# Performance work log

Measured on AMD Instinct MI355X. Metric: run time of the kernel, lower is better.

The kernel has to match this reference:

```python
import jax, jax.numpy as jnp
import numpy as np

N_HEADS = 12
C = 3          # per-head in/hidden/out channels (12/4)
C_PRED = 1     # predictor hidden (4/4)
BN_EPS = 1e-5
COS_EPS = 1e-8
B, H, W = 8, 512, 768


def setup_inputs() -> dict:
    key = jax.random.key(0)
    ks = jax.random.split(key, 22)
    p = lambda k, s: jax.random.normal(k, s, jnp.float32) * 0.1
    return {
        "latent1": jax.random.normal(ks[0], (B, N_HEADS, H, W), jnp.float32),
        "latent2": jax.random.normal(ks[1], (B, N_HEADS, H, W), jnp.float32),
        # projector conv1 + BN
        "W1": p(ks[2], (N_HEADS, C, C)), "b1": p(ks[3], (N_HEADS, C)),
        "g1": 1.0 + p(ks[4], (N_HEADS, C)), "be1": p(ks[5], (N_HEADS, C)),
        # projector conv2 + BN
        "W2": p(ks[6], (N_HEADS, C, C)), "b2": p(ks[7], (N_HEADS, C)),
        "g2": 1.0 + p(ks[8], (N_HEADS, C)), "be2": p(ks[9], (N_HEADS, C)),
        # projector conv3 + BN (no ReLU)
        "W3": p(ks[10], (N_HEADS, C, C)), "b3": p(ks[11], (N_HEADS, C)),
        "g3": 1.0 + p(ks[12], (N_HEADS, C)), "be3": p(ks[13], (N_HEADS, C)),
        # predictor conv1 + BN
        "W4": p(ks[14], (N_HEADS, C_PRED, C)), "b4": p(ks[15], (N_HEADS, C_PRED)),
        "g4": 1.0 + p(ks[16], (N_HEADS, C_PRED)), "be4": p(ks[17], (N_HEADS, C_PRED)),
        # predictor conv2 (no BN)
        "W5": p(ks[18], (N_HEADS, C, C_PRED)), "b5": p(ks[19], (N_HEADS, C)),
    }


def _conv1x1(x, Wk, bk):
    # x: [B, Cin, H, W'], Wk: [Cout, Cin]
    return jnp.einsum('oc,bchw->bohw', Wk, x) + bk[None, :, None, None]


def _bn(x, g, be):
    # training-mode BatchNorm2d: batch statistics over (B, H, W)
    m = x.mean(axis=(0, 2, 3), keepdims=True)
    v = x.var(axis=(0, 2, 3), keepdims=True)  # biased var, as torch BN uses
    return (x - m) * jax.lax.rsqrt(v + BN_EPS) * g[None, :, None, None] + be[None, :, None, None]


def _cos_loss(p, z):
    # -mean(cosine_similarity(p, detach(z), dim=1))
    z = jax.lax.stop_gradient(z)
    dot = jnp.sum(p * z, axis=1)
    npn = jnp.maximum(jnp.sqrt(jnp.sum(p * p, axis=1)), COS_EPS)
    nzn = jnp.maximum(jnp.sqrt(jnp.sum(z * z, axis=1)), COS_EPS)
    return -jnp.mean(dot / (npn * nzn))


def _head_loss(x1, x2, W1, b1, g1, be1, W2, b2, g2, be2, W3, b3, g3, be3,
               W4, b4, g4, be4, W5, b5):
    def proj(x):
        x = jax.nn.relu(_bn(_conv1x1(x, W1, b1), g1, be1))
        x = jax.nn.relu(_bn(_conv1x1(x, W2, b2), g2, be2))
        return _bn(_conv1x1(x, W3, b3), g3, be3)

    def pred(z):
        h = jax.nn.relu(_bn(_conv1x1(z, W4, b4), g4, be4))
        return _conv1x1(h, W5, b5)

    z1, z2 = proj(x1), proj(x2)
    p1, p2 = pred(z1), pred(z2)
    return 0.5 * (_cos_loss(p1, z2) + _cos_loss(p2, z1))


def reference(latent1, latent2, W1, b1, g1, be1, W2, b2, g2, be2,
              W3, b3, g3, be3, W4, b4, g4, be4, W5, b5):
    Bd, Cd, Hd, Wd = latent1.shape
    Wp = Wd // C
    # per-channel view [B, H, W] -> [B, 3, H, W/3]; stack heads on leading axis
    x1 = latent1.reshape(Bd, N_HEADS, C, Hd, Wp).transpose(1, 0, 2, 3, 4)
    x2 = latent2.reshape(Bd, N_HEADS, C, Hd, Wp).transpose(1, 0, 2, 3, 4)
    losses = jax.vmap(_head_loss)(x1, x2, W1, b1, g1, be1, W2, b2, g2, be2,
                                  W3, b3, g3, be3, W4, b4, g4, be4, W5, b5)
    return jnp.sum(losses)
```

## Files before the change

### kernel.cpp

```cpp
#include <hip/hip_runtime.h>
#include <hip/hip_fp16.h>
#include <math.h>


typedef unsigned short ushort_t;
typedef unsigned int   uint_t;

constexpr int   NH      = 12;
constexpr int   POS     = 131072;
constexpr int   NB      = 8;
constexpr long long MLL = (long long)NB * POS;
constexpr int   CSPAN   = POS / 16;
constexpr int   SBLK    = 128;
constexpr int   NTOT    = NB * NH * 3 * POS;

constexpr size_t XH_BYTES   = (size_t)NTOT * 2;
constexpr size_t P_CNT      = (size_t)24 * SBLK * 9;
constexpr size_t DBL_COUNT  = 3 * P_CNT + (size_t)12 * SBLK;
constexpr size_t NEED_BYTES = 2 * XH_BYTES + DBL_COUNT * 8 + (size_t)24 * 40 * 4;

template <int K>
__device__ inline void block_reduce_to0(double (&v)[K]) {
#pragma unroll
  for (int off = 32; off > 0; off >>= 1) {
#pragma unroll
    for (int k = 0; k < K; ++k) v[k] += __shfl_down(v[k], off, 64);
  }
  __shared__ double lds[4][K];
  const int lane = threadIdx.x & 63;
  const int wv   = threadIdx.x >> 6;
  if (lane == 0) {
#pragma unroll
    for (int k = 0; k < K; ++k) lds[wv][k] = v[k];
  }
  __syncthreads();
  if (threadIdx.x == 0) {
#pragma unroll
    for (int k = 0; k < K; ++k) v[k] = lds[0][k] + lds[1][k] + lds[2][k] + lds[3][k];
  }
}

__device__ inline uint_t pack2h(float lo, float hi) {
  return (uint_t)__half_as_ushort(__float2half(lo)) |
         ((uint_t)__half_as_ushort(__float2half(hi)) << 16);
}
__device__ inline float h_lo(uint_t w) {
  return __half2float(__ushort_as_half((unsigned short)(w & 0xFFFFu)));
}
__device__ inline float h_hi(uint_t w) {
  return __half2float(__ushort_as_half((unsigned short)(w >> 16)));
}

template <bool H16>
__device__ inline void load3x8(const float* __restrict__ X,
                               const ushort_t* __restrict__ XH,
                               size_t e, float (&f)[3][8]) {
#pragma unroll
  for (int c = 0; c < 3; ++c) {
    const size_t a = e + (size_t)c * POS;
    if constexpr (H16) {
      const uint4 v = *(const uint4*)(XH + a);
      f[c][0] = h_lo(v.x); f[c][1] = h_hi(v.x);
      f[c][2] = h_lo(v.y); f[c][3] = h_hi(v.y);
      f[c][4] = h_lo(v.z); f[c][5] = h_hi(v.z);
      f[c][6] = h_lo(v.w); f[c][7] = h_hi(v.w);
    } else {
      const float4 u0 = *(const float4*)(X + a);
      const float4 u1 = *(const float4*)(X + a + 4);
      f[c][0] = u0.x; f[c][1] = u0.y; f[c][2] = u0.z; f[c][3] = u0.w;
      f[c][4] = u1.x; f[c][5] = u1.y; f[c][6] = u1.z; f[c][7] = u1.w;
    }
  }
}

__device__ inline void store8h(ushort_t* __restrict__ XH, size_t e,
                               const float (&g)[8]) {
  uint4 h;
  h.x = pack2h(g[0], g[1]);
  h.y = pack2h(g[2], g[3]);
  h.z = pack2h(g[4], g[5]);
  h.w = pack2h(g[6], g[7]);
  *(uint4*)(XH + e) = h;
}

template <bool STORE>
__global__ __launch_bounds__(256) void passA1_kernel(
    const float* __restrict__ x1, const float* __restrict__ x2,
    ushort_t* __restrict__ xh1, ushort_t* __restrict__ xh2,
    double* __restrict__ P0) {
  const int u = blockIdx.y;
  const int s = u % 24;
  const int b = u / 24;
  const int n = s >> 1;
  const float* __restrict__ X = (s & 1) ? x2 : x1;
  ushort_t* __restrict__ XH = (s & 1) ? xh2 : xh1;
  const size_t off0 = (size_t)((b * NH + n) * 3) * POS + (size_t)blockIdx.x * CSPAN;

  float acc[9] = {0.f, 0.f, 0.f, 0.f, 0.f, 0.f, 0.f, 0.f, 0.f};
#pragma unroll 2
  for (int i = 0; i < 4; ++i) {
    const size_t e = off0 + i * 2048 + threadIdx.x * 8;
    float f[3][8];
    load3x8<false>(X, nullptr, e, f);
    if constexpr (STORE) {
#pragma unroll
      for (int c = 0; c < 3; ++c) store8h(XH, e + (size_t)c * POS, f[c]);
    }
#pragma unroll
    for (int j = 0; j < 8; ++j) {
      const float X0 = f[0][j], X1 = f[1][j], X2 = f[2][j];
      acc[0] += X0;      acc[1] += X1;      acc[2] += X2;
      acc[3] += X0 * X0; acc[4] += X1 * X1; acc[5] += X2 * X2;
      acc[6] += X0 * X1; acc[7] += X0 * X2; acc[8] += X1 * X2;
    }
  }

  double v9[9];
#pragma unroll
  for (int k = 0; k < 9; ++k) v9[k] = (double)acc[k];
  block_reduce_to0<9>(v9);
  if (threadIdx.x == 0) {
    double* dst = P0 + ((size_t)s * SBLK + b * 16 + blockIdx.x) * 9;
#pragma unroll
    for (int k = 0; k < 9; ++k) dst[k] = v9[k];
  }
}

__device__ inline void moments_to_mc(const double (&v)[9], double (&m)[3],
                                     double (&C)[3][3]) {
  const double M = (double)MLL;
  m[0] = v[0] / M; m[1] = v[1] / M; m[2] = v[2] / M;
  C[0][0] = v[3] / M - m[0] * m[0];
  C[1][1] = v[4] / M - m[1] * m[1];
  C[2][2] = v[5] / M - m[2] * m[2];
  C[0][1] = C[1][0] = v[6] / M - m[0] * m[1];
  C[0][2] = C[2][0] = v[7] / M - m[0] * m[2];
  C[1][2] = C[2][1] = v[8] / M - m[1] * m[2];
}

__global__ __launch_bounds__(256) void stats_fold_kernel(
    const double* __restrict__ P, const float* __restrict__ Wk,
    const float* __restrict__ bk, const float* __restrict__ gk,
    const float* __restrict__ bek, float* __restrict__ derived, int outoff) {
  const int s = blockIdx.x;
  const int t = threadIdx.x;
  const int n = s >> 1;
  double v[9] = {0, 0, 0, 0, 0, 0, 0, 0, 0};
  if (t < SBLK) {
    const double* p = P + ((size_t)s * SBLK + t) * 9;
#pragma unroll
    for (int k = 0; k < 9; ++k) v[k] = p[k];
  }
  block_reduce_to0<9>(v);
  if (t == 0) {
    double m[3], C[3][3];
    moments_to_mc(v, m, C);
    for (int o = 0; o < 3; ++o) {
      const double w0 = Wk[n * 9 + o * 3 + 0];
      const double w1 = Wk[n * 9 + o * 3 + 1];
      const double w2 = Wk[n * 9 + o * 3 + 2];
      const double my = w0 * m[0] + w1 * m[1] + w2 * m[2] + (double)bk[n * 3 + o];
      const double vy = w0 * w0 * C[0][0] + w1 * w1 * C[1][1] + w2 * w2 * C[2][2] +
                        2.0 * (w0 * w1 * C[0][1] + w0 * w2 * C[0][2] + w1 * w2 * C[1][2]);
      const double sc = (double)gk[n * 3 + o] / sqrt(vy + 1e-5);
      const double tt = (double)bek[n * 3 + o] - my * sc;
      derived[s * 40 + outoff + o * 3 + 0] = (float)(sc * w0);
      derived[s * 40 + outoff + o * 3 + 1] = (float)(sc * w1);
      derived[s * 40 + outoff + o * 3 + 2] = (float)(sc * w2);
      derived[s * 40 + outoff + 9 + o]     = (float)(sc * (double)bk[n * 3 + o] + tt);
    }
  }
}

template <bool H16>
__global__ __launch_bounds__(256) void passA2_kernel(
    const float* __restrict__ x1, const float* __restrict__ x2,
    ushort_t* __restrict__ xh1, ushort_t* __restrict__ xh2,
    const float* __restrict__ derived, double* __restrict__ P1) {
  const int u = blockIdx.y;
  const int s = u % 24;
  const int b = u / 24;
  const int n = s >> 1;
  const float* __restrict__ X = (s & 1) ? x2 : x1;
  ushort_t* __restrict__ XH = (s & 1) ? xh2 : xh1;
  const size_t off0 = (size_t)((b * NH + n) * 3) * POS + (size_t)blockIdx.x * CSPAN;

  const float* D = derived + s * 40;
  float w1f[3][3], c1v[3];
#pragma unroll
  for (int o = 0; o < 3; ++o) {
#pragma unroll
    for (int c = 0; c < 3; ++c) w1f[o][c] = D[o * 3 + c];
    c1v[o] = D[9 + o];
  }

  float acc[9] = {0.f, 0.f, 0.f, 0.f, 0.f, 0.f, 0.f, 0.f, 0.f};
#pragma unroll 2
  for (int i = 0; i < 4; ++i) {
    const size_t e = off0 + i * 2048 + threadIdx.x * 8;
    float f[3][8];
    load3x8<H16>(X, XH, e, f);
    float A[3][8];
#pragma unroll
    for (int j = 0; j < 8; ++j) {
      const float X0 = f[0][j], X1 = f[1][j], X2 = f[2][j];
#pragma unroll
      for (int o = 0; o < 3; ++o)
        A[o][j] = fmaxf(0.f, fmaf(w1f[o][0], X0,
                         fmaf(w1f[o][1], X1, fmaf(w1f[o][2], X2, c1v[o]))));
      const float A0 = A[0][j], A1 = A[1][j], A2v = A[2][j];
      acc[0] += A0;       acc[1] += A1;       acc[2] += A2v;
      acc[3] += A0 * A0;  acc[4] += A1 * A1;  acc[5] += A2v * A2v;
      acc[6] += A0 * A1;  acc[7] += A0 * A2v; acc[8] += A1 * A2v;
    }
    if constexpr (H16) {
#pragma unroll
      for (int c = 0; c < 3; ++c) store8h(XH, e + (size_t)c * POS, A[c]);
    }
  }

  double v9[9];
#pragma unroll
  for (int k = 0; k < 9; ++k) v9[k] = (double)acc[k];
  block_reduce_to0<9>(v9);
  if (threadIdx.x == 0) {
    double* dst = P1 + ((size_t)s * SBLK + b * 16 + blockIdx.x) * 9;
#pragma unroll
    for (int k = 0; k < 9; ++k) dst[k] = v9[k];
  }
}

template <bool H16>
__global__ __launch_bounds__(256) void passC2_kernel(
    const float* __restrict__ x1, const float* __restrict__ x2,
    ushort_t* __restrict__ xh1, ushort_t* __restrict__ xh2,
    const float* __restrict__ derived, double* __restrict__ P2) {
  const int u = blockIdx.y;
  const int s = u % 24;
  const int b = u / 24;
  const int n = s >> 1;
  const float* __restrict__ X = (s & 1) ? x2 : x1;
  ushort_t* __restrict__ XH = (s & 1) ? xh2 : xh1;
  const size_t off0 = (size_t)((b * NH + n) * 3) * POS + (size_t)blockIdx.x * CSPAN;

  const float* D = derived + s * 40;
  float w1f[3][3], c1v[3];
  if constexpr (!H16) {
#pragma unroll
    for (int o = 0; o < 3; ++o) {
#pragma unroll
      for (int c = 0; c < 3; ++c) w1f[o][c] = D[o * 3 + c];
      c1v[o] = D[9 + o];
    }
  }
  float w2f[3][3], c2v[3];
#pragma unroll
  for (int o = 0; o < 3; ++o) {
#pragma unroll
    for (int c = 0; c < 3; ++c) w2f[o][c] = D[12 + o * 3 + c];
    c2v[o] = D[21 + o];
  }

  float acc[9] = {0.f, 0.f, 0.f, 0.f, 0.f, 0.f, 0.f, 0.f, 0.f};
#pragma unroll 2
  for (int i = 0; i < 4; ++i) {
    const size_t e = off0 + i * 2048 + threadIdx.x * 8;
    float f[3][8];
    load3x8<H16>(X, XH, e, f);
    float A[3][8];
#pragma unroll
    for (int j = 0; j < 8; ++j) {
      float a0, a1, a2;
      if constexpr (H16) {
        a0 = f[0][j]; a1 = f[1][j]; a2 = f[2][j];
      } else {
        const float X0 = f[0][j], X1 = f[1][j], X2 = f[2][j];
        a0 = fmaxf(0.f, fmaf(w1f[0][0], X0, fmaf(w1f[0][1], X1, fmaf(w1f[0][2], X2, c1v[0]))));
        a1 = fmaxf(0.f, fmaf(w1f[1][0], X0, fmaf(w1f[1][1], X1, fmaf(w1f[1][2], X2, c1v[1]))));
        a2 = fmaxf(0.f, fmaf(w1f[2][0], X0, fmaf(w1f[2][1], X1, fmaf(w1f[2][2], X2, c1v[2]))));
      }
#pragma unroll
      for (int o = 0; o < 3; ++o)
        A[o][j] = fmaxf(0.f, fmaf(w2f[o][0], a0,
                         fmaf(w2f[o][1], a1, fmaf(w2f[o][2], a2, c2v[o]))));
      const float A0 = A[0][j], A1 = A[1][j], A2v = A[2][j];
      acc[0] += A0;       acc[1] += A1;       acc[2] += A2v;
      acc[3] += A0 * A0;  acc[4] += A1 * A1;  acc[5] += A2v * A2v;
      acc[6] += A0 * A1;  acc[7] += A0 * A2v; acc[8] += A1 * A2v;
    }
    if constexpr (H16) {
#pragma unroll
      for (int c = 0; c < 3; ++c) store8h(XH, e + (size_t)c * POS, A[c]);
    }
  }

  double v9[9];
#pragma unroll
  for (int k = 0; k < 9; ++k) v9[k] = (double)acc[k];
  block_reduce_to0<9>(v9);
  if (threadIdx.x == 0) {
    double* dst = P2 + ((size_t)s * SBLK + b * 16 + blockIdx.x) * 9;
#pragma unroll
    for (int k = 0; k < 9; ++k) dst[k] = v9[k];
  }
}

__global__ __launch_bounds__(256) void statsC2_kernel(
    const double* __restrict__ P2, const float* __restrict__ W3,
    const float* __restrict__ b3, const float* __restrict__ g3,
    const float* __restrict__ be3, const float* __restrict__ W4,
    const float* __restrict__ b4, const float* __restrict__ g4,
    const float* __restrict__ be4, float* __restrict__ derived) {
  const int s = blockIdx.x;
  const int t = threadIdx.x;
  const int n = s >> 1;
  double v[9] = {0, 0, 0, 0, 0, 0, 0, 0, 0};
  if (t < SBLK) {
    const double* p = P2 + ((size_t)s * SBLK + t) * 9;
#pragma unroll
    for (int k = 0; k < 9; ++k) v[k] = p[k];
  }
  block_reduce_to0<9>(v);
  if (t == 0) {
    double m[3], C[3][3];
    moments_to_mc(v, m, C);
    double F3d[3][3], c3d[3];
    for (int o = 0; o < 3; ++o) {
      const double w0 = W3[n * 9 + o * 3 + 0];
      const double w1 = W3[n * 9 + o * 3 + 1];
      const double w2 = W3[n * 9 + o * 3 + 2];
      const double m3 = w0 * m[0] + w1 * m[1] + w2 * m[2] + (double)b3[n * 3 + o];
      const double vy = w0 * w0 * C[0][0] + w1 * w1 * C[1][1] + w2 * w2 * C[2][2] +
                        2.0 * (w0 * w1 * C[0][1] + w0 * w2 * C[0][2] + w1 * w2 * C[1][2]);
      const double s3 = (double)g3[n * 3 + o] / sqrt(vy + 1e-5);
      const double t3 = (double)be3[n * 3 + o] - m3 * s3;
      F3d[o][0] = s3 * w0; F3d[o][1] = s3 * w1; F3d[o][2] = s3 * w2;
      c3d[o] = s3 * (double)b3[n * 3 + o] + t3;
      derived[s * 40 + 24 + o * 3 + 0] = (float)F3d[o][0];
      derived[s * 40 + 24 + o * 3 + 1] = (float)F3d[o][1];
      derived[s * 40 + 24 + o * 3 + 2] = (float)F3d[o][2];
      derived[s * 40 + 33 + o]         = (float)c3d[o];
    }
    double q[3] = {0.0, 0.0, 0.0};
    double d = (double)b4[n];
    for (int o = 0; o < 3; ++o) {
      const double w4o = W4[n * 3 + o];
      q[0] += w4o * F3d[o][0];
      q[1] += w4o * F3d[o][1];
      q[2] += w4o * F3d[o][2];
      d += w4o * c3d[o];
    }
    const double m4 = q[0] * m[0] + q[1] * m[1] + q[2] * m[2] + d;
    double v4 = 0.0;
    for (int i2 = 0; i2 < 3; ++i2)
      for (int j2 = 0; j2 < 3; ++j2) v4 += q[i2] * q[j2] * C[i2][j2];
    const double s4 = (double)g4[n] / sqrt(v4 + 1e-5);
    const double t4 = (double)be4[n] - m4 * s4;
    for (int o = 0; o < 3; ++o)
      derived[s * 40 + 36 + o] = (float)(s4 * (double)W4[n * 3 + o]);
    derived[s * 40 + 39] = (float)(s4 * (double)b4[n] + t4);
  }
}

template <bool H16>
__device__ inline void tail_chain(
    const float (&F1)[3][3], const float (&C1)[3],
    const float (&F2)[3][3], const float (&C2)[3],
    const float (&F3)[3][3], const float (&C3)[3],
    const float (&W4s)[3], float B4c,
    const float (&w5)[3], const float (&b5v)[3],
    float v0, float v1, float v2, float (&z)[3], float (&p)[3]) {
  float a0 = v0, a1 = v1, a2 = v2;
  if constexpr (!H16) {
    const float t0 = fmaxf(0.f, fmaf(F1[0][0], v0, fmaf(F1[0][1], v1, fmaf(F1[0][2], v2, C1[0]))));
    const float t1 = fmaxf(0.f, fmaf(F1[1][0], v0, fmaf(F1[1][1], v1, fmaf(F1[1][2], v2, C1[1]))));
    const float t2 = fmaxf(0.f, fmaf(F1[2][0], v0, fmaf(F1[2][1], v1, fmaf(F1[2][2], v2, C1[2]))));
    a0 = fmaxf(0.f, fmaf(F2[0][0], t0, fmaf(F2[0][1], t1, fmaf(F2[0][2], t2, C2[0]))));
    a1 = fmaxf(0.f, fmaf(F2[1][0], t0, fmaf(F2[1][1], t1, fmaf(F2[1][2], t2, C2[1]))));
    a2 = fmaxf(0.f, fmaf(F2[2][0], t0, fmaf(F2[2][1], t1, fmaf(F2[2][2], t2, C2[2]))));
  }
#pragma unroll
  for (int o = 0; o < 3; ++o)
    z[o] = fmaf(F3[o][0], a0, fmaf(F3[o][1], a1, fmaf(F3[o][2], a2, C3[o])));
  const float y4 = fmaf(W4s[0], z[0], fmaf(W4s[1], z[1], fmaf(W4s[2], z[2], B4c)));
  const float h = fmaxf(0.f, y4);
#pragma unroll
  for (int o = 0; o < 3; ++o) p[o] = fmaf(w5[o], h, b5v[o]);
}

template <bool H16>
__global__ __launch_bounds__(256) void passD2_kernel(
    const float* __restrict__ x1, const float* __restrict__ x2,
    const ushort_t* __restrict__ xh1, const ushort_t* __restrict__ xh2,
    const float* __restrict__ W5, const float* __restrict__ b5,
    const float* __restrict__ derived, double* __restrict__ PL) {
  const int u = blockIdx.y;
  const int n = u % 12;
  const int b = u / 12;
  const size_t off0 = (size_t)((b * NH + n) * 3) * POS + (size_t)blockIdx.x * CSPAN;

  float F1[2][3][3], C1[2][3], F2[2][3][3], C2[2][3];
  float F3[2][3][3], C3[2][3], W4s[2][3], B4c[2];
#pragma unroll
  for (int br = 0; br < 2; ++br) {
    const float* D = derived + (size_t)(2 * n + br) * 40;
    if constexpr (!H16) {
#pragma unroll
      for (int o = 0; o < 3; ++o) {
#pragma unroll
        for (int c = 0; c < 3; ++c) {
          F1[br][o][c] = D[o * 3 + c];
          F2[br][o][c] = D[12 + o * 3 + c];
        }
        C1[br][o] = D[9 + o];
        C2[br][o] = D[21 + o];
      }
    }
#pragma unroll
    for (int o = 0; o < 3; ++o) {
#pragma unroll
      for (int c = 0; c < 3; ++c) F3[br][o][c] = D[24 + o * 3 + c];
      C3[br][o]  = D[33 + o];
      W4s[br][o] = D[36 + o];
    }
    B4c[br] = D[39];
  }
  float w5[3], b5v[3];
#pragma unroll
  for (int o = 0; o < 3; ++o) {
    w5[o]  = W5[n * 3 + o];
    b5v[o] = b5[n * 3 + o];
  }

  float acc = 0.f;
  for (int i = 0; i < 4; ++i) {
    const size_t e = off0 + i * 2048 + threadIdx.x * 8;
    float fA[3][8], fB[3][8];
    load3x8<H16>(x1, xh1, e, fA);
    load3x8<H16>(x2, xh2, e, fB);
#pragma unroll
    for (int j = 0; j < 8; ++j) {
      float z1[3], p1[3], z2[3], p2[3];
      tail_chain<H16>(F1[0], C1[0], F2[0], C2[0], F3[0], C3[0], W4s[0], B4c[0],
                      w5, b5v, fA[0][j], fA[1][j], fA[2][j], z1, p1);
      tail_chain<H16>(F1[1], C1[1], F2[1], C2[1], F3[1], C3[1], W4s[1], B4c[1],
                      w5, b5v, fB[0][j], fB[1][j], fB[2][j], z2, p2);

      const float d12 = p1[0] * z2[0] + p1[1] * z2[1] + p1[2] * z2[2];
      const float pp1 = p1[0] * p1[0] + p1[1] * p1[1] + p1[2] * p1[2];
      const float zz2 = z2[0] * z2[0] + z2[1] * z2[1] + z2[2] * z2[2];
      acc += d12 * __builtin_amdgcn_rsqf(fmaxf(pp1, 1e-16f)) *
                   __builtin_amdgcn_rsqf(fmaxf(zz2, 1e-16f));

      const float d21 = p2[0] * z1[0] + p2[1] * z1[1] + p2[2] * z1[2];
      const float pp2 = p2[0] * p2[0] + p2[1] * p2[1] + p2[2] * p2[2];
      const float zz1 = z1[0] * z1[0] + z1[1] * z1[1] + z1[2] * z1[2];
      acc += d21 * __builtin_amdgcn_rsqf(fmaxf(pp2, 1e-16f)) *
                   __builtin_amdgcn_rsqf(fmaxf(zz1, 1e-16f));
    }
  }

  double v[1] = {(double)acc};
  block_reduce_to0<1>(v);
  if (threadIdx.x == 0) PL[(size_t)n * SBLK + b * 16 + blockIdx.x] = v[0];
}

__global__ __launch_bounds__(256) void finalize_kernel(
    const double* __restrict__ PL, float* __restrict__ out) {
  double v[1] = {0.0};
  for (int k = threadIdx.x; k < 12 * SBLK; k += 256) v[0] += PL[k];
  block_reduce_to0<1>(v);
  if (threadIdx.x == 0) out[0] = (float)(-0.5 * v[0] / (double)MLL);
}

extern "C" void kernel_launch(void* const* d_in, const int* in_sizes, int n_in,
                              void* d_out, int out_size, void* d_ws, size_t ws_size,
                              hipStream_t stream) {
  const float* x1  = (const float*)d_in[0];
  const float* x2  = (const float*)d_in[1];
  const float* W1  = (const float*)d_in[2];
  const float* b1  = (const float*)d_in[3];
  const float* g1  = (const float*)d_in[4];
  const float* be1 = (const float*)d_in[5];
  const float* W2  = (const float*)d_in[6];
  const float* b2  = (const float*)d_in[7];
  const float* g2  = (const float*)d_in[8];
  const float* be2 = (const float*)d_in[9];
  const float* W3  = (const float*)d_in[10];
  const float* b3  = (const float*)d_in[11];
  const float* g3  = (const float*)d_in[12];
  const float* be3 = (const float*)d_in[13];
  const float* W4  = (const float*)d_in[14];
  const float* b4  = (const float*)d_in[15];
  const float* g4  = (const float*)d_in[16];
  const float* be4 = (const float*)d_in[17];
  const float* W5  = (const float*)d_in[18];
  const float* b5  = (const float*)d_in[19];

  const bool big = ws_size >= NEED_BYTES;
  ushort_t* xh1 = nullptr;
  ushort_t* xh2 = nullptr;
  double* dbase;
  if (big) {
    xh1 = (ushort_t*)d_ws;
    xh2 = xh1 + NTOT;
    dbase = (double*)(xh2 + NTOT);
  } else {
    dbase = (double*)d_ws;
  }
  double* P0 = dbase;
  double* P1 = P0 + P_CNT;
  double* P2 = P1 + P_CNT;
  double* PL = P2 + P_CNT;
  float* derived = (float*)(PL + 12 * SBLK);

  const dim3 blk(256);
  const dim3 gA(16, 192);
  const dim3 gD(16, 96);

  if (big) {
    passA1_kernel<true><<<gA, blk, 0, stream>>>(x1, x2, xh1, xh2, P0);
    stats_fold_kernel<<<24, blk, 0, stream>>>(P0, W1, b1, g1, be1, derived, 0);
    passA2_kernel<true><<<gA, blk, 0, stream>>>(x1, x2, xh1, xh2, derived, P1);
    stats_fold_kernel<<<24, blk, 0, stream>>>(P1, W2, b2, g2, be2, derived, 12);
    passC2_kernel<true><<<gA, blk, 0, stream>>>(x1, x2, xh1, xh2, derived, P2);
    statsC2_kernel<<<24, blk, 0, stream>>>(P2, W3, b3, g3, be3, W4, b4, g4, be4,
                                           derived);
    passD2_kernel<true><<<gD, blk, 0, stream>>>(x1, x2, xh1, xh2, W5, b5,
                                                derived, PL);
  } else {
    passA1_kernel<false><<<gA, blk, 0, stream>>>(x1, x2, nullptr, nullptr, P0);
    stats_fold_kernel<<<24, blk, 0, stream>>>(P0, W1, b1, g1, be1, derived, 0);
    passA2_kernel<false><<<gA, blk, 0, stream>>>(x1, x2, nullptr, nullptr,
                                                 derived, P1);
    stats_fold_kernel<<<24, blk, 0, stream>>>(P1, W2, b2, g2, be2, derived, 12);
    passC2_kernel<false><<<gA, blk, 0, stream>>>(x1, x2, nullptr, nullptr,
                                                 derived, P2);
    statsC2_kernel<<<24, blk, 0, stream>>>(P2, W3, b3, g3, be3, W4, b4, g4, be4,
                                           derived);
    passD2_kernel<false><<<gD, blk, 0, stream>>>(x1, x2, nullptr, nullptr, W5, b5,
                                                 derived, PL);
  }
  finalize_kernel<<<1, blk, 0, stream>>>(PL, (float*)d_out);
}
```

Measured before the change: 505.8 us.

## Fold BN statistics into pass prologues and drop intermediate fp16 activation writes

Removes the separate stats-fold kernels and the finalize kernel. Each pass now reduces the previous per-block moment partials and computes the folded BN affine in its own prologue, and the last pass accumulates the loss with atomics plus a last-block counter. Later passes no longer write fp16 intermediate activations; they recompute the full chain from the fp16 copy of the input. This trades fewer launches and less write traffic for redundant prologue reductions in every block and extra ALU work recomputing earlier layers.

```diff
diff --git a/kernel.cpp b/kernel.cpp
--- a/kernel.cpp
+++ b/kernel.cpp
@@ -14,10 +14,8 @@
 constexpr int   SBLK    = 128;
 constexpr int   NTOT    = NB * NH * 3 * POS;
 
-constexpr size_t XH_BYTES   = (size_t)NTOT * 2;
 constexpr size_t P_CNT      = (size_t)24 * SBLK * 9;
-constexpr size_t DBL_COUNT  = 3 * P_CNT + (size_t)12 * SBLK;
-constexpr size_t NEED_BYTES = 2 * XH_BYTES + DBL_COUNT * 8 + (size_t)24 * 40 * 4;
+constexpr size_t NEED_BYTES = (size_t)NTOT * 2 * 2 + 3 * P_CNT * 8 + 64;
 
 template <int K>
 __device__ inline void block_reduce_to0(double (&v)[K]) {
@@ -27,6 +25,7 @@
     for (int k = 0; k < K; ++k) v[k] += __shfl_down(v[k], off, 64);
   }
   __shared__ double lds[4][K];
+  __syncthreads();
   const int lane = threadIdx.x & 63;
   const int wv   = threadIdx.x >> 6;
   if (lane == 0) {
@@ -83,49 +82,6 @@
   *(uint4*)(XH + e) = h;
 }
 
-template <bool STORE>
-__global__ __launch_bounds__(256) void passA1_kernel(
-    const float* __restrict__ x1, const float* __restrict__ x2,
-    ushort_t* __restrict__ xh1, ushort_t* __restrict__ xh2,
-    double* __restrict__ P0) {
-  const int u = blockIdx.y;
-  const int s = u % 24;
-  const int b = u / 24;
-  const int n = s >> 1;
-  const float* __restrict__ X = (s & 1) ? x2 : x1;
-  ushort_t* __restrict__ XH = (s & 1) ? xh2 : xh1;
-  const size_t off0 = (size_t)((b * NH + n) * 3) * POS + (size_t)blockIdx.x * CSPAN;
-
-  float acc[9] = {0.f, 0.f, 0.f, 0.f, 0.f, 0.f, 0.f, 0.f, 0.f};
-#pragma unroll 2
-  for (int i = 0; i < 4; ++i) {
-    const size_t e = off0 + i * 2048 + threadIdx.x * 8;
-    float f[3][8];
-    load3x8<false>(X, nullptr, e, f);
-    if constexpr (STORE) {
-#pragma unroll
-      for (int c = 0; c < 3; ++c) store8h(XH, e + (size_t)c * POS, f[c]);
-    }
-#pragma unroll
-    for (int j = 0; j < 8; ++j) {
-      const float X0 = f[0][j], X1 = f[1][j], X2 = f[2][j];
-      acc[0] += X0;      acc[1] += X1;      acc[2] += X2;
-      acc[3] += X0 * X0; acc[4] += X1 * X1; acc[5] += X2 * X2;
-      acc[6] += X0 * X1; acc[7] += X0 * X2; acc[8] += X1 * X2;
-    }
-  }
-
-  double v9[9];
-#pragma unroll
-  for (int k = 0; k < 9; ++k) v9[k] = (double)acc[k];
-  block_reduce_to0<9>(v9);
-  if (threadIdx.x == 0) {
-    double* dst = P0 + ((size_t)s * SBLK + b * 16 + blockIdx.x) * 9;
-#pragma unroll
-    for (int k = 0; k < 9; ++k) dst[k] = v9[k];
-  }
-}
-
 __device__ inline void moments_to_mc(const double (&v)[9], double (&m)[3],
                                      double (&C)[3][3]) {
   const double M = (double)MLL;
@@ -138,45 +94,98 @@
   C[1][2] = C[2][1] = v[8] / M - m[1] * m[2];
 }
 
-__global__ __launch_bounds__(256) void stats_fold_kernel(
-    const double* __restrict__ P, const float* __restrict__ Wk,
-    const float* __restrict__ bk, const float* __restrict__ gk,
-    const float* __restrict__ bek, float* __restrict__ derived, int outoff) {
-  const int s = blockIdx.x;
-  const int t = threadIdx.x;
-  const int n = s >> 1;
-  double v[9] = {0, 0, 0, 0, 0, 0, 0, 0, 0};
-  if (t < SBLK) {
-    const double* p = P + ((size_t)s * SBLK + t) * 9;
+__device__ inline void slice_reduce9(const double* __restrict__ P, int s,
+                                     double (&v)[9]) {
+#pragma unroll
+  for (int k = 0; k < 9; ++k) v[k] = 0.0;
+  if (threadIdx.x < SBLK) {
+    const double* p = P + ((size_t)s * SBLK + threadIdx.x) * 9;
 #pragma unroll
     for (int k = 0; k < 9; ++k) v[k] = p[k];
   }
   block_reduce_to0<9>(v);
-  if (t == 0) {
-    double m[3], C[3][3];
-    moments_to_mc(v, m, C);
-    for (int o = 0; o < 3; ++o) {
-      const double w0 = Wk[n * 9 + o * 3 + 0];
-      const double w1 = Wk[n * 9 + o * 3 + 1];
-      const double w2 = Wk[n * 9 + o * 3 + 2];
-      const double my = w0 * m[0] + w1 * m[1] + w2 * m[2] + (double)bk[n * 3 + o];
-      const double vy = w0 * w0 * C[0][0] + w1 * w1 * C[1][1] + w2 * w2 * C[2][2] +
-                        2.0 * (w0 * w1 * C[0][1] + w0 * w2 * C[0][2] + w1 * w2 * C[1][2]);
-      const double sc = (double)gk[n * 3 + o] / sqrt(vy + 1e-5);
-      const double tt = (double)bek[n * 3 + o] - my * sc;
-      derived[s * 40 + outoff + o * 3 + 0] = (float)(sc * w0);
-      derived[s * 40 + outoff + o * 3 + 1] = (float)(sc * w1);
-      derived[s * 40 + outoff + o * 3 + 2] = (float)(sc * w2);
-      derived[s * 40 + outoff + 9 + o]     = (float)(sc * (double)bk[n * 3 + o] + tt);
-    }
-  }
-}
-
-template <bool H16>
-__global__ __launch_bounds__(256) void passA2_kernel(
+}
+
+__device__ inline void fold_math(const double (&v)[9], const float* __restrict__ Wk,
+                                 const float* __restrict__ bk,
+                                 const float* __restrict__ gk,
+                                 const float* __restrict__ bek, int n,
+                                 float* __restrict__ dst) {
+  double m[3], C[3][3];
+  moments_to_mc(v, m, C);
+  for (int o = 0; o < 3; ++o) {
+    const double w0 = Wk[n * 9 + o * 3 + 0];
+    const double w1 = Wk[n * 9 + o * 3 + 1];
+    const double w2 = Wk[n * 9 + o * 3 + 2];
+    const double my = w0 * m[0] + w1 * m[1] + w2 * m[2] + (double)bk[n * 3 + o];
+    const double vy = w0 * w0 * C[0][0] + w1 * w1 * C[1][1] + w2 * w2 * C[2][2] +
+                      2.0 * (w0 * w1 * C[0][1] + w0 * w2 * C[0][2] + w1 * w2 * C[1][2]);
+    const double sc = (double)gk[n * 3 + o] / sqrt(vy + 1e-5);
+    const double tt = (double)bek[n * 3 + o] - my * sc;
+    dst[o * 3 + 0] = (float)(sc * w0);
+    dst[o * 3 + 1] = (float)(sc * w1);
+    dst[o * 3 + 2] = (float)(sc * w2);
+    dst[9 + o]     = (float)(sc * (double)bk[n * 3 + o] + tt);
+  }
+}
+
+__device__ inline void fold34_math(const double (&v)[9], const float* __restrict__ W3,
+                                   const float* __restrict__ b3,
+                                   const float* __restrict__ g3,
+                                   const float* __restrict__ be3,
+                                   const float* __restrict__ W4,
+                                   const float* __restrict__ b4,
+                                   const float* __restrict__ g4,
+                                   const float* __restrict__ be4, int n,
+                                   float* __restrict__ dst) {
+  double m[3], C[3][3];
+  moments_to_mc(v, m, C);
+  double F3d[3][3], c3d[3];
+  for (int o = 0; o < 3; ++o) {
+    const double w0 = W3[n * 9 + o * 3 + 0];
+    const double w1 = W3[n * 9 + o * 3 + 1];
+    const double w2 = W3[n * 9 + o * 3 + 2];
+    const double m3 = w0 * m[0] + w1 * m[1] + w2 * m[2] + (double)b3[n * 3 + o];
+    const double vy = w0 * w0 * C[0][0] + w1 * w1 * C[1][1] + w2 * w2 * C[2][2] +
+                      2.0 * (w0 * w1 * C[0][1] + w0 * w2 * C[0][2] + w1 * w2 * C[1][2]);
+    const double s3 = (double)g3[n * 3 + o] / sqrt(vy + 1e-5);
+    const double t3 = (double)be3[n * 3 + o] - m3 * s3;
+    F3d[o][0] = s3 * w0; F3d[o][1] = s3 * w1; F3d[o][2] = s3 * w2;
+    c3d[o] = s3 * (double)b3[n * 3 + o] + t3;
+    dst[o * 3 + 0] = (float)F3d[o][0];
+    dst[o * 3 + 1] = (float)F3d[o][1];
+    dst[o * 3 + 2] = (float)F3d[o][2];
+    dst[9 + o]     = (float)c3d[o];
+  }
+  double q[3] = {0.0, 0.0, 0.0};
+  double d = (double)b4[n];
+  for (int o = 0; o < 3; ++o) {
+    const double w4o = W4[n * 3 + o];
+    q[0] += w4o * F3d[o][0];
+    q[1] += w4o * F3d[o][1];
+    q[2] += w4o * F3d[o][2];
+    d += w4o * c3d[o];
+  }
+  const double m4 = q[0] * m[0] + q[1] * m[1] + q[2] * m[2] + d;
+  double v4 = 0.0;
+  for (int i = 0; i < 3; ++i)
+    for (int j = 0; j < 3; ++j) v4 += q[i] * q[j] * C[i][j];
+  const double s4 = (double)g4[n] / sqrt(v4 + 1e-5);
+  const double t4 = (double)be4[n] - m4 * s4;
+  for (int o = 0; o < 3; ++o) dst[12 + o] = (float)(s4 * (double)W4[n * 3 + o]);
+  dst[15] = (float)(s4 * (double)b4[n] + t4);
+}
+
+template <bool STORE>
+__global__ __launch_bounds__(256) void pass1_kernel(
     const float* __restrict__ x1, const float* __restrict__ x2,
     ushort_t* __restrict__ xh1, ushort_t* __restrict__ xh2,
-    const float* __restrict__ derived, double* __restrict__ P1) {
+    double* __restrict__ P0, double* __restrict__ lossAcc,
+    uint_t* __restrict__ cnt) {
+  if (blockIdx.x == 0 && blockIdx.y == 0 && threadIdx.x == 0) {
+    *lossAcc = 0.0;
+    *cnt = 0u;
+  }
   const int u = blockIdx.y;
   const int s = u % 24;
   const int b = u / 24;
@@ -185,13 +194,63 @@
   ushort_t* __restrict__ XH = (s & 1) ? xh2 : xh1;
   const size_t off0 = (size_t)((b * NH + n) * 3) * POS + (size_t)blockIdx.x * CSPAN;
 
-  const float* D = derived + s * 40;
+  float acc[9] = {0.f, 0.f, 0.f, 0.f, 0.f, 0.f, 0.f, 0.f, 0.f};
+#pragma unroll 2
+  for (int i = 0; i < 4; ++i) {
+    const size_t e = off0 + i * 2048 + threadIdx.x * 8;
+    float f[3][8];
+    load3x8<false>(X, nullptr, e, f);
+    if constexpr (STORE) {
+#pragma unroll
+      for (int c = 0; c < 3; ++c) store8h(XH, e + (size_t)c * POS, f[c]);
+    }
+#pragma unroll
+    for (int j = 0; j < 8; ++j) {
+      const float X0 = f[0][j], X1 = f[1][j], X2 = f[2][j];
+      acc[0] += X0;      acc[1] += X1;      acc[2] += X2;
+      acc[3] += X0 * X0; acc[4] += X1 * X1; acc[5] += X2 * X2;
+      acc[6] += X0 * X1; acc[7] += X0 * X2; acc[8] += X1 * X2;
+    }
+  }
+  double v9[9];
+#pragma unroll
+  for (int k = 0; k < 9; ++k) v9[k] = (double)acc[k];
+  block_reduce_to0<9>(v9);
+  if (threadIdx.x == 0) {
+    double* dst = P0 + ((size_t)s * SBLK + b * 16 + blockIdx.x) * 9;
+#pragma unroll
+    for (int k = 0; k < 9; ++k) dst[k] = v9[k];
+  }
+}
+
+template <bool H16>
+__global__ __launch_bounds__(256) void pass2_kernel(
+    const float* __restrict__ x1, const float* __restrict__ x2,
+    const ushort_t* __restrict__ xh1, const ushort_t* __restrict__ xh2,
+    const float* __restrict__ W1, const float* __restrict__ b1,
+    const float* __restrict__ g1, const float* __restrict__ be1,
+    const double* __restrict__ P0, double* __restrict__ P1) {
+  const int u = blockIdx.y;
+  const int s = u % 24;
+  const int b = u / 24;
+  const int n = s >> 1;
+  const float* __restrict__ X = (s & 1) ? x2 : x1;
+  const ushort_t* __restrict__ XH = (s & 1) ? xh2 : xh1;
+  const size_t off0 = (size_t)((b * NH + n) * 3) * POS + (size_t)blockIdx.x * CSPAN;
+
+  __shared__ float sf1[12];
+  {
+    double v[9];
+    slice_reduce9(P0, s, v);
+    if (threadIdx.x == 0) fold_math(v, W1, b1, g1, be1, n, sf1);
+    __syncthreads();
+  }
   float w1f[3][3], c1v[3];
 #pragma unroll
   for (int o = 0; o < 3; ++o) {
 #pragma unroll
-    for (int c = 0; c < 3; ++c) w1f[o][c] = D[o * 3 + c];
-    c1v[o] = D[9 + o];
+    for (int c = 0; c < 3; ++c) w1f[o][c] = sf1[o * 3 + c];
+    c1v[o] = sf1[9 + o];
   }
 
   float acc[9] = {0.f, 0.f, 0.f, 0.f, 0.f, 0.f, 0.f, 0.f, 0.f};
@@ -200,25 +259,17 @@
     const size_t e = off0 + i * 2048 + threadIdx.x * 8;
     float f[3][8];
     load3x8<H16>(X, XH, e, f);
-    float A[3][8];
 #pragma unroll
     for (int j = 0; j < 8; ++j) {
       const float X0 = f[0][j], X1 = f[1][j], X2 = f[2][j];
-#pragma unroll
-      for (int o = 0; o < 3; ++o)
-        A[o][j] = fmaxf(0.f, fmaf(w1f[o][0], X0,
-                         fmaf(w1f[o][1], X1, fmaf(w1f[o][2], X2, c1v[o]))));
-      const float A0 = A[0][j], A1 = A[1][j], A2v = A[2][j];
+      const float A0 = fmaxf(0.f, fmaf(w1f[0][0], X0, fmaf(w1f[0][1], X1, fmaf(w1f[0][2], X2, c1v[0]))));
+      const float A1 = fmaxf(0.f, fmaf(w1f[1][0], X0, fmaf(w1f[1][1], X1, fmaf(w1f[1][2], X2, c1v[1]))));
+      const float A2v= fmaxf(0.f, fmaf(w1f[2][0], X0, fmaf(w1f[2][1], X1, fmaf(w1f[2][2], X2, c1v[2]))));
       acc[0] += A0;       acc[1] += A1;       acc[2] += A2v;
       acc[3] += A0 * A0;  acc[4] += A1 * A1;  acc[5] += A2v * A2v;
       acc[6] += A0 * A1;  acc[7] += A0 * A2v; acc[8] += A1 * A2v;
     }
-    if constexpr (H16) {
-#pragma unroll
-      for (int c = 0; c < 3; ++c) store8h(XH, e + (size_t)c * POS, A[c]);
-    }
-  }
-
+  }
   double v9[9];
 #pragma unroll
   for (int k = 0; k < 9; ++k) v9[k] = (double)acc[k];
@@ -231,34 +282,42 @@
 }
 
 template <bool H16>
-__global__ __launch_bounds__(256) void passC2_kernel(
+__global__ __launch_bounds__(256) void pass3_kernel(
     const float* __restrict__ x1, const float* __restrict__ x2,
-    ushort_t* __restrict__ xh1, ushort_t* __restrict__ xh2,
-    const float* __restrict__ derived, double* __restrict__ P2) {
+    const ushort_t* __restrict__ xh1, const ushort_t* __restrict__ xh2,
+    const float* __restrict__ W1, const float* __restrict__ b1,
+    const float* __restrict__ g1, const float* __restrict__ be1,
+    const float* __restrict__ W2, const float* __restrict__ b2,
+    const float* __restrict__ g2, const float* __restrict__ be2,
+    const double* __restrict__ P0, const double* __restrict__ P1,
+    double* __restrict__ P2) {
   const int u = blockIdx.y;
   const int s = u % 24;
   const int b = u / 24;
   const int n = s >> 1;
   const float* __restrict__ X = (s & 1) ? x2 : x1;
-  ushort_t* __restrict__ XH = (s & 1) ? xh2 : xh1;
+  const ushort_t* __restrict__ XH = (s & 1) ? xh2 : xh1;
   const size_t off0 = (size_t)((b * NH + n) * 3) * POS + (size_t)blockIdx.x * CSPAN;
 
-  const float* D = derived + s * 40;
-  float w1f[3][3], c1v[3];
-  if constexpr (!H16) {
-#pragma unroll
-    for (int o = 0; o < 3; ++o) {
-#pragma unroll
-      for (int c = 0; c < 3; ++c) w1f[o][c] = D[o * 3 + c];
-      c1v[o] = D[9 + o];
-    }
-  }
-  float w2f[3][3], c2v[3];
+  __shared__ float sf1[12], sf2[12];
+  {
+    double v[9];
+    slice_reduce9(P0, s, v);
+    if (threadIdx.x == 0) fold_math(v, W1, b1, g1, be1, n, sf1);
+    slice_reduce9(P1, s, v);
+    if (threadIdx.x == 0) fold_math(v, W2, b2, g2, be2, n, sf2);
+    __syncthreads();
+  }
+  float w1f[3][3], c1v[3], w2f[3][3], c2v[3];
 #pragma unroll
   for (int o = 0; o < 3; ++o) {
 #pragma unroll
-    for (int c = 0; c < 3; ++c) w2f[o][c] = D[12 + o * 3 + c];
-    c2v[o] = D[21 + o];
+    for (int c = 0; c < 3; ++c) {
+      w1f[o][c] = sf1[o * 3 + c];
+      w2f[o][c] = sf2[o * 3 + c];
+    }
+    c1v[o] = sf1[9 + o];
+    c2v[o] = sf2[9 + o];
   }
 
   float acc[9] = {0.f, 0.f, 0.f, 0.f, 0.f, 0.f, 0.f, 0.f, 0.f};
@@ -267,33 +326,20 @@
     const size_t e = off0 + i * 2048 + threadIdx.x * 8;
     float f[3][8];
     load3x8<H16>(X, XH, e, f);
-    float A[3][8];
 #pragma unroll
     for (int j = 0; j < 8; ++j) {
-      float a0, a1, a2;
-      if constexpr (H16) {
-        a0 = f[0][j]; a1 = f[1][j]; a2 = f[2][j];
-      } else {
-        const float X0 = f[0][j], X1 = f[1][j], X2 = f[2][j];
-        a0 = fmaxf(0.f, fmaf(w1f[0][0], X0, fmaf(w1f[0][1], X1, fmaf(w1f[0][2], X2, c1v[0]))));
-        a1 = fmaxf(0.f, fmaf(w1f[1][0], X0, fmaf(w1f[1][1], X1, fmaf(w1f[1][2], X2, c1v[1]))));
-        a2 = fmaxf(0.f, fmaf(w1f[2][0], X0, fmaf(w1f[2][1], X1, fmaf(w1f[2][2], X2, c1v[2]))));
-      }
-#pragma unroll
-      for (int o = 0; o < 3; ++o)
-        A[o][j] = fmaxf(0.f, fmaf(w2f[o][0], a0,
-                         fmaf(w2f[o][1], a1, fmaf(w2f[o][2], a2, c2v[o]))));
-      const float A0 = A[0][j], A1 = A[1][j], A2v = A[2][j];
+      const float X0 = f[0][j], X1 = f[1][j], X2 = f[2][j];
+      const float a0 = fmaxf(0.f, fmaf(w1f[0][0], X0, fmaf(w1f[0][1], X1, fmaf(w1f[0][2], X2, c1v[0]))));
+      const float a1 = fmaxf(0.f, fmaf(w1f[1][0], X0, fmaf(w1f[1][1], X1, fmaf(w1f[1][2], X2, c1v[1]))));
+      const float a2 = fmaxf(0.f, fmaf(w1f[2][0], X0, fmaf(w1f[2][1], X1, fmaf(w1f[2][2], X2, c1v[2]))));
+      const float A0 = fmaxf(0.f, fmaf(w2f[0][0], a0, fmaf(w2f[0][1], a1, fmaf(w2f[0][2], a2, c2v[0]))));
+      const float A1 = fmaxf(0.f, fmaf(w2f[1][0], a0, fmaf(w2f[1][1], a1, fmaf(w2f[1][2], a2, c2v[1]))));
+      const float A2v= fmaxf(0.f, fmaf(w2f[2][0], a0, fmaf(w2f[2][1], a1, fmaf(w2f[2][2], a2, c2v[2]))));
       acc[0] += A0;       acc[1] += A1;       acc[2] += A2v;
       acc[3] += A0 * A0;  acc[4] += A1 * A1;  acc[5] += A2v * A2v;
       acc[6] += A0 * A1;  acc[7] += A0 * A2v; acc[8] += A1 * A2v;
     }
-    if constexpr (H16) {
-#pragma unroll
-      for (int c = 0; c < 3; ++c) store8h(XH, e + (size_t)c * POS, A[c]);
-    }
-  }
-
+  }
   double v9[9];
 #pragma unroll
   for (int k = 0; k < 9; ++k) v9[k] = (double)acc[k];
@@ -305,125 +351,66 @@
   }
 }
 
-__global__ __launch_bounds__(256) void statsC2_kernel(
-    const double* __restrict__ P2, const float* __restrict__ W3,
-    const float* __restrict__ b3, const float* __restrict__ g3,
-    const float* __restrict__ be3, const float* __restrict__ W4,
-    const float* __restrict__ b4, const float* __restrict__ g4,
-    const float* __restrict__ be4, float* __restrict__ derived) {
-  const int s = blockIdx.x;
-  const int t = threadIdx.x;
-  const int n = s >> 1;
-  double v[9] = {0, 0, 0, 0, 0, 0, 0, 0, 0};
-  if (t < SBLK) {
-    const double* p = P2 + ((size_t)s * SBLK + t) * 9;
-#pragma unroll
-    for (int k = 0; k < 9; ++k) v[k] = p[k];
-  }
-  block_reduce_to0<9>(v);
-  if (t == 0) {
-    double m[3], C[3][3];
-    moments_to_mc(v, m, C);
-    double F3d[3][3], c3d[3];
-    for (int o = 0; o < 3; ++o) {
-      const double w0 = W3[n * 9 + o * 3 + 0];
-      const double w1 = W3[n * 9 + o * 3 + 1];
-      const double w2 = W3[n * 9 + o * 3 + 2];
-      const double m3 = w0 * m[0] + w1 * m[1] + w2 * m[2] + (double)b3[n * 3 + o];
-      const double vy = w0 * w0 * C[0][0] + w1 * w1 * C[1][1] + w2 * w2 * C[2][2] +
-                        2.0 * (w0 * w1 * C[0][1] + w0 * w2 * C[0][2] + w1 * w2 * C[1][2]);
-      const double s3 = (double)g3[n * 3 + o] / sqrt(vy + 1e-5);
-      const double t3 = (double)be3[n * 3 + o] - m3 * s3;
-      F3d[o][0] = s3 * w0; F3d[o][1] = s3 * w1; F3d[o][2] = s3 * w2;
-      c3d[o] = s3 * (double)b3[n * 3 + o] + t3;
-      derived[s * 40 + 24 + o * 3 + 0] = (float)F3d[o][0];
-      derived[s * 40 + 24 + o * 3 + 1] = (float)F3d[o][1];
-      derived[s * 40 + 24 + o * 3 + 2] = (float)F3d[o][2];
-      derived[s * 40 + 33 + o]         = (float)c3d[o];
-    }
-    double q[3] = {0.0, 0.0, 0.0};
-    double d = (double)b4[n];
-    for (int o = 0; o < 3; ++o) {
-      const double w4o = W4[n * 3 + o];
-      q[0] += w4o * F3d[o][0];
-      q[1] += w4o * F3d[o][1];
-      q[2] += w4o * F3d[o][2];
-      d += w4o * c3d[o];
-    }
-    const double m4 = q[0] * m[0] + q[1] * m[1] + q[2] * m[2] + d;
-    double v4 = 0.0;
-    for (int i2 = 0; i2 < 3; ++i2)
-      for (int j2 = 0; j2 < 3; ++j2) v4 += q[i2] * q[j2] * C[i2][j2];
-    const double s4 = (double)g4[n] / sqrt(v4 + 1e-5);
-    const double t4 = (double)be4[n] - m4 * s4;
-    for (int o = 0; o < 3; ++o)
-      derived[s * 40 + 36 + o] = (float)(s4 * (double)W4[n * 3 + o]);
-    derived[s * 40 + 39] = (float)(s4 * (double)b4[n] + t4);
-  }
+__device__ inline void full_chain(const float (&S)[40], const float (&w5)[3],
+                                  const float (&b5v)[3], float v0, float v1,
+                                  float v2, float (&z)[3], float (&p)[3]) {
+  const float t0 = fmaxf(0.f, fmaf(S[0], v0, fmaf(S[1], v1, fmaf(S[2], v2, S[9]))));
+  const float t1 = fmaxf(0.f, fmaf(S[3], v0, fmaf(S[4], v1, fmaf(S[5], v2, S[10]))));
+  const float t2 = fmaxf(0.f, fmaf(S[6], v0, fmaf(S[7], v1, fmaf(S[8], v2, S[11]))));
+  const float a0 = fmaxf(0.f, fmaf(S[12], t0, fmaf(S[13], t1, fmaf(S[14], t2, S[21]))));
+  const float a1 = fmaxf(0.f, fmaf(S[15], t0, fmaf(S[16], t1, fmaf(S[17], t2, S[22]))));
+  const float a2 = fmaxf(0.f, fmaf(S[18], t0, fmaf(S[19], t1, fmaf(S[20], t2, S[23]))));
+  z[0] = fmaf(S[24], a0, fmaf(S[25], a1, fmaf(S[26], a2, S[33])));
+  z[1] = fmaf(S[27], a0, fmaf(S[28], a1, fmaf(S[29], a2, S[34])));
+  z[2] = fmaf(S[30], a0, fmaf(S[31], a1, fmaf(S[32], a2, S[35])));
+  const float y4 = fmaf(S[36], z[0], fmaf(S[37], z[1], fmaf(S[38], z[2], S[39])));
+  const float h = fmaxf(0.f, y4);
+#pragma unroll
+  for (int o = 0; o < 3; ++o) p[o] = fmaf(w5[o], h, b5v[o]);
 }
 
 template <bool H16>
-__device__ inline void tail_chain(
-    const float (&F1)[3][3], const float (&C1)[3],
-    const float (&F2)[3][3], const float (&C2)[3],
-    const float (&F3)[3][3], const float (&C3)[3],
-    const float (&W4s)[3], float B4c,
-    const float (&w5)[3], const float (&b5v)[3],
-    float v0, float v1, float v2, float (&z)[3], float (&p)[3]) {
-  float a0 = v0, a1 = v1, a2 = v2;
-  if constexpr (!H16) {
-    const float t0 = fmaxf(0.f, fmaf(F1[0][0], v0, fmaf(F1[0][1], v1, fmaf(F1[0][2], v2, C1[0]))));
-    const float t1 = fmaxf(0.f, fmaf(F1[1][0], v0, fmaf(F1[1][1], v1, fmaf(F1[1][2], v2, C1[1]))));
-    const float t2 = fmaxf(0.f, fmaf(F1[2][0], v0, fmaf(F1[2][1], v1, fmaf(F1[2][2], v2, C1[2]))));
-    a0 = fmaxf(0.f, fmaf(F2[0][0], t0, fmaf(F2[0][1], t1, fmaf(F2[0][2], t2, C2[0]))));
-    a1 = fmaxf(0.f, fmaf(F2[1][0], t0, fmaf(F2[1][1], t1, fmaf(F2[1][2], t2, C2[1]))));
-    a2 = fmaxf(0.f, fmaf(F2[2][0], t0, fmaf(F2[2][1], t1, fmaf(F2[2][2], t2, C2[2]))));
-  }
-#pragma unroll
-  for (int o = 0; o < 3; ++o)
-    z[o] = fmaf(F3[o][0], a0, fmaf(F3[o][1], a1, fmaf(F3[o][2], a2, C3[o])));
-  const float y4 = fmaf(W4s[0], z[0], fmaf(W4s[1], z[1], fmaf(W4s[2], z[2], B4c)));
-  const float h = fmaxf(0.f, y4);
-#pragma unroll
-  for (int o = 0; o < 3; ++o) p[o] = fmaf(w5[o], h, b5v[o]);
-}
-
-template <bool H16>
-__global__ __launch_bounds__(256) void passD2_kernel(
+__global__ __launch_bounds__(256) void pass4_kernel(
     const float* __restrict__ x1, const float* __restrict__ x2,
     const ushort_t* __restrict__ xh1, const ushort_t* __restrict__ xh2,
+    const float* __restrict__ W1, const float* __restrict__ b1,
+    const float* __restrict__ g1, const float* __restrict__ be1,
+    const float* __restrict__ W2, const float* __restrict__ b2,
+    const float* __restrict__ g2, const float* __restrict__ be2,
+    const float* __restrict__ W3, const float* __restrict__ b3,
+    const float* __restrict__ g3, const float* __restrict__ be3,
+    const float* __restrict__ W4, const float* __restrict__ b4,
+    const float* __restrict__ g4, const float* __restrict__ be4,
     const float* __restrict__ W5, const float* __restrict__ b5,
-    const float* __restrict__ derived, double* __restrict__ PL) {
+    const double* __restrict__ P0, const double* __restrict__ P1,
+    const double* __restrict__ P2, double* __restrict__ lossAcc,
+    uint_t* __restrict__ cnt, float* __restrict__ out) {
   const int u = blockIdx.y;
   const int n = u % 12;
   const int b = u / 12;
   const size_t off0 = (size_t)((b * NH + n) * 3) * POS + (size_t)blockIdx.x * CSPAN;
 
-  float F1[2][3][3], C1[2][3], F2[2][3][3], C2[2][3];
-  float F3[2][3][3], C3[2][3], W4s[2][3], B4c[2];
-#pragma unroll
-  for (int br = 0; br < 2; ++br) {
-    const float* D = derived + (size_t)(2 * n + br) * 40;
-    if constexpr (!H16) {
-#pragma unroll
-      for (int o = 0; o < 3; ++o) {
-#pragma unroll
-        for (int c = 0; c < 3; ++c) {
-          F1[br][o][c] = D[o * 3 + c];
-          F2[br][o][c] = D[12 + o * 3 + c];
-        }
-        C1[br][o] = D[9 + o];
-        C2[br][o] = D[21 + o];
-      }
-    }
-#pragma unroll
-    for (int o = 0; o < 3; ++o) {
-#pragma unroll
-      for (int c = 0; c < 3; ++c) F3[br][o][c] = D[24 + o * 3 + c];
-      C3[br][o]  = D[33 + o];
-      W4s[br][o] = D[36 + o];
-    }
-    B4c[br] = D[39];
+  __shared__ float sh[2][40];
+  {
+    double v[9];
+#pragma unroll
+    for (int br = 0; br < 2; ++br) {
+      const int s = 2 * n + br;
+      slice_reduce9(P0, s, v);
+      if (threadIdx.x == 0) fold_math(v, W1, b1, g1, be1, n, &sh[br][0]);
+      slice_reduce9(P1, s, v);
+      if (threadIdx.x == 0) fold_math(v, W2, b2, g2, be2, n, &sh[br][12]);
+      slice_reduce9(P2, s, v);
+      if (threadIdx.x == 0)
+        fold34_math(v, W3, b3, g3, be3, W4, b4, g4, be4, n, &sh[br][24]);
+    }
+    __syncthreads();
+  }
+  float S0[40], S1[40];
+#pragma unroll
+  for (int k = 0; k < 40; ++k) {
+    S0[k] = sh[0][k];
+    S1[k] = sh[1][k];
   }
   float w5[3], b5v[3];
 #pragma unroll
@@ -441,10 +428,8 @@
 #pragma unroll
     for (int j = 0; j < 8; ++j) {
       float z1[3], p1[3], z2[3], p2[3];
-      tail_chain<H16>(F1[0], C1[0], F2[0], C2[0], F3[0], C3[0], W4s[0], B4c[0],
-                      w5, b5v, fA[0][j], fA[1][j], fA[2][j], z1, p1);
-      tail_chain<H16>(F1[1], C1[1], F2[1], C2[1], F3[1], C3[1], W4s[1], B4c[1],
-                      w5, b5v, fB[0][j], fB[1][j], fB[2][j], z2, p2);
+      full_chain(S0, w5, b5v, fA[0][j], fA[1][j], fA[2][j], z1, p1);
+      full_chain(S1, w5, b5v, fB[0][j], fB[1][j], fB[2][j], z2, p2);
 
       const float d12 = p1[0] * z2[0] + p1[1] * z2[1] + p1[2] * z2[2];
       const float pp1 = p1[0] * p1[0] + p1[1] * p1[1] + p1[2] * p1[2];
@@ -462,15 +447,17 @@
 
   double v[1] = {(double)acc};
   block_reduce_to0<1>(v);
-  if (threadIdx.x == 0) PL[(size_t)n * SBLK + b * 16 + blockIdx.x] = v[0];
-}
-
-__global__ __launch_bounds__(256) void finalize_kernel(
-    const double* __restrict__ PL, float* __restrict__ out) {
-  double v[1] = {0.0};
-  for (int k = threadIdx.x; k < 12 * SBLK; k += 256) v[0] += PL[k];
-  block_reduce_to0<1>(v);
-  if (threadIdx.x == 0) out[0] = (float)(-0.5 * v[0] / (double)MLL);
+  if (threadIdx.x == 0) {
+    atomicAdd(lossAcc, v[0]);
+    __threadfence();
+    const uint_t total = gridDim.x * gridDim.y;
+    const uint_t old = atomicAdd(cnt, 1u);
+    if (old == total - 1u) {
+      __threadfence();
+      const double tot = atomicAdd(lossAcc, 0.0);
+      out[0] = (float)(-0.5 * tot / (double)MLL);
+    }
+  }
 }
 
 extern "C" void kernel_launch(void* const* d_in, const int* in_sizes, int n_in,
@@ -511,35 +498,35 @@
   double* P0 = dbase;
   double* P1 = P0 + P_CNT;
   double* P2 = P1 + P_CNT;
-  double* PL = P2 + P_CNT;
-  float* derived = (float*)(PL + 12 * SBLK);
+  double* lossAcc = P2 + P_CNT;
+  uint_t* cnt = (uint_t*)(lossAcc + 1);
 
   const dim3 blk(256);
   const dim3 gA(16, 192);
   const dim3 gD(16, 96);
 
   if (big) {
-    passA1_kernel<true><<<gA, blk, 0, stream>>>(x1, x2, xh1, xh2, P0);
-    stats_fold_kernel<<<24, blk, 0, stream>>>(P0, W1, b1, g1, be1, derived, 0);
-    passA2_kernel<true><<<gA, blk, 0, stream>>>(x1, x2, xh1, xh2, derived, P1);
-    stats_fold_kernel<<<24, blk, 0, stream>>>(P1, W2, b2, g2, be2, derived, 12);
-    passC2_kernel<true><<<gA, blk, 0, stream>>>(x1, x2, xh1, xh2, derived, P2);
-    statsC2_kernel<<<24, blk, 0, stream>>>(P2, W3, b3, g3, be3, W4, b4, g4, be4,
-                                           derived);
-    passD2_kernel<true><<<gD, blk, 0, stream>>>(x1, x2, xh1, xh2, W5, b5,
-                                                derived, PL);
+    pass1_kernel<true><<<gA, blk, 0, stream>>>(x1, x2, xh1, xh2, P0, lossAcc, cnt);
+    pass2_kernel<true><<<gA, blk, 0, stream>>>(x1, x2, xh1, xh2, W1, b1, g1, be1,
+                                               P0, P1);
+    pass3_kernel<true><<<gA, blk, 0, stream>>>(x1, x2, xh1, xh2, W1, b1, g1, be1,
+                                               W2, b2, g2, be2, P0, P1, P2);
+    pass4_kernel<true><<<gD, blk, 0, stream>>>(x1, x2, xh1, xh2, W1, b1, g1, be1,
+                                               W2, b2, g2, be2, W3, b3, g3, be3,
+                                               W4, b4, g4, be4, W5, b5, P0, P1,
+                                               P2, lossAcc, cnt, (float*)d_out);
   } else {
-    passA1_kernel<false><<<gA, blk, 0, stream>>>(x1, x2, nullptr, nullptr, P0);
-    stats_fold_kernel<<<24, blk, 0, stream>>>(P0, W1, b1, g1, be1, derived, 0);
-    passA2_kernel<false><<<gA, blk, 0, stream>>>(x1, x2, nullptr, nullptr,
-                                                 derived, P1);
-    stats_fold_kernel<<<24, blk, 0, stream>>>(P1, W2, b2, g2, be2, derived, 12);
-    passC2_kernel<false><<<gA, blk, 0, stream>>>(x1, x2, nullptr, nullptr,
-                                                 derived, P2);
-    statsC2_kernel<<<24, blk, 0, stream>>>(P2, W3, b3, g3, be3, W4, b4, g4, be4,
-                                           derived);
-    passD2_kernel<false><<<gD, blk, 0, stream>>>(x1, x2, nullptr, nullptr, W5, b5,
-                                                 derived, PL);
-  }
-  finalize_kernel<<<1, blk, 0, stream>>>(PL, (float*)d_out);
-}
+    pass1_kernel<false><<<gA, blk, 0, stream>>>(x1, x2, nullptr, nullptr, P0,
+                                                lossAcc, cnt);
+    pass2_kernel<false><<<gA, blk, 0, stream>>>(x1, x2, nullptr, nullptr, W1, b1,
+                                                g1, be1, P0, P1);
+    pass3_kernel<false><<<gA, blk, 0, stream>>>(x1, x2, nullptr, nullptr, W1, b1,
+                                                g1, be1, W2, b2, g2, be2, P0, P1,
+                                                P2);
+    pass4_kernel<false><<<gD, blk, 0, stream>>>(x1, x2, nullptr, nullptr, W1, b1,
+                                                g1, be1, W2, b2, g2, be2, W3, b3,
+                                                g3, be3, W4, b4, g4, be4, W5, b5,
+                                                P0, P1, P2, lossAcc, cnt,
+                                                (float*)d_out);
+  }
+}
```

Measured after the change: 580.4 us. 14.8% more time.
